# Kernel tuning notes

Measured on AMD Instinct MI355X. Metric: run time of the kernel, lower is better.

The kernel has to match this reference:

```python
import jax, jax.numpy as jnp
import numpy as np

B, T, M, D = 2, 2048, 2048, 128
H = M // D
ROTARY_BASE = 10000
NORM_EPS = 1e-6
QK_SCALE = 1.0 / D  # mult = sqrt(qk_scale) applied to both q and k
INFTY_APPROX = 1e30


def setup_inputs() -> dict:
    key = jax.random.key(0)
    ks = jax.random.split(key, 6)
    w_scale = M ** (-0.5)
    return {
        "x": jax.random.normal(ks[0], (B, T, M), jnp.float32),
        "wq": jax.random.normal(ks[1], (M, H, D), jnp.float32) * w_scale,
        "wk": jax.random.normal(ks[2], (M, H, D), jnp.float32) * w_scale,
        "wv": jax.random.normal(ks[3], (M, H, D), jnp.float32) * w_scale,
        "wo": jax.random.normal(ks[4], (H, D, M), jnp.float32) * w_scale,
        "gq": jnp.zeros((H, 1, D), jnp.float32),
        "bq": jnp.zeros((H, 1, D), jnp.float32),
        "gk": jnp.zeros((H, 1, D), jnp.float32),
        "bk": jnp.zeros((H, 1, D), jnp.float32),
    }


def _qk_layernorm(x, g, b):
    # x: [B,H,T,D]; g,b: [H,1,D]; centered RMS norm with trainable (1+g), b
    x = x - jnp.mean(x, axis=-1, keepdims=True)
    x = x / jnp.sqrt(jnp.mean(jnp.square(x), axis=-1, keepdims=True) + NORM_EPS)
    return x * (1.0 + g)[None] + b[None]


def _rotary(x):
    # x: [B,H,T,D]; half-split rotary encoding
    half = D // 2
    positions = jnp.arange(T, dtype=jnp.float32)[:, None]          # [T,1]
    ang_freqs = jnp.power(float(ROTARY_BASE), -jnp.arange(half, dtype=jnp.float32) / half)[None, :]  # [1,half]
    radians = positions * ang_freqs                                  # [T,half]
    cos = jnp.cos(radians)[None, None].astype(x.dtype)               # [1,1,T,half]
    sin = jnp.sin(radians)[None, None].astype(x.dtype)
    even, odd = jnp.split(x, 2, axis=-1)
    return jnp.concatenate([even * cos - odd * sin, even * sin + odd * cos], axis=-1)


def reference(x, wq, wk, wv, wo, gq, bq, gk, bk):
    q = jnp.einsum('bim,mhd->bhid', x, wq)
    k = jnp.einsum('bim,mhd->bhid', x, wk)
    v = jnp.einsum('bim,mhd->bhid', x, wv)
    q = _rotary(_qk_layernorm(q, gq, bq))
    k = _rotary(_qk_layernorm(k, gk, bk))
    mult = jnp.asarray(QK_SCALE ** 0.5, dtype=x.dtype)
    s = jnp.einsum('bhid,bhjd->bhij', q * mult, k * mult)            # [B,H,T,T]
    i = jnp.arange(T)[:, None]
    j = jnp.arange(T)[None, :]
    future = (i < j)[None, None]                                      # mask future positions
    s = s - jnp.asarray(INFTY_APPROX, dtype=s.dtype) * future
    p = jax.nn.softmax(s, axis=-1)
    o = jnp.einsum('bhij,bhjd->bhid', p, v)
    return jnp.einsum('bhid,hdm->bim', o, wo)
```

## Files before the change

### kernel.cpp

```cpp
#include <hip/hip_runtime.h>


#define NB 2
#define NT 2048
#define NM 2048
#define NH 16
#define ND 128

typedef __attribute__((ext_vector_type(4))) float f32x4;
typedef __attribute__((ext_vector_type(8))) short bf16x8;
typedef __attribute__((ext_vector_type(4))) short bf16x4;

#define AS1 __attribute__((address_space(1)))
#define AS3 __attribute__((address_space(3)))

__device__ __forceinline__ unsigned short f2bf(float f){
  unsigned int u = __float_as_uint(f);
  u = (u + 0x7fffu + ((u >> 16) & 1u)) >> 16;
  return (unsigned short)u;
}
__device__ __forceinline__ float bf2f(short s){
  return __uint_as_float(((unsigned int)(unsigned short)s) << 16);
}
__device__ __forceinline__ float wredsum(float v){
  #pragma unroll
  for (int m = 1; m < 64; m <<= 1) v += __shfl_xor(v, m);
  return v;
}
__device__ __forceinline__ void gload_lds16(const void* g, void* l){
  __builtin_amdgcn_global_load_lds((const AS1 void*)g, (AS3 void*)l, 16, 0, 0);
}

__global__ __launch_bounds__(64) void rope_table_k(float* ctab, float* stab){
  int t = blockIdx.x, i = threadIdx.x;
  float freq = __expf(-(float)i * (9.210340371976184f / 64.0f));
  float ang = (float)t * freq;
  ctab[t * 64 + i] = cosf(ang);
  stab[t * 64 + i] = sinf(ang);
}

__global__ __launch_bounds__(256) void cast_x_k(const float* __restrict__ x,
                                                short* __restrict__ xb){
  size_t gid = (size_t)blockIdx.x * 256 + threadIdx.x;
  float4 v = *(const float4*)(x + gid * 4);
  bf16x4 o;
  o[0] = (short)f2bf(v.x); o[1] = (short)f2bf(v.y);
  o[2] = (short)f2bf(v.z); o[3] = (short)f2bf(v.w);
  *(bf16x4*)(xb + gid * 4) = o;
}

__global__ __launch_bounds__(256) void transpose_w_k(const float* __restrict__ wq,
                                                     const float* __restrict__ wk,
                                                     const float* __restrict__ wv,
                                                     const float* __restrict__ wo,
                                                     short* __restrict__ wT){
  __shared__ float tl[32][33];
  int z = blockIdx.z;
  const float* src = (z == 0) ? wq : (z == 1) ? wk : (z == 2) ? wv : wo;
  short* dst = wT + (size_t)z * 2048 * 2048;
  int n0 = blockIdx.x * 32, k0 = blockIdx.y * 32;
  int cx = threadIdx.x & 31, ry = threadIdx.x >> 5;
  #pragma unroll
  for (int p = 0; p < 4; ++p)
    tl[ry + 8 * p][cx] = src[(size_t)(k0 + ry + 8 * p) * 2048 + n0 + cx];
  __syncthreads();
  #pragma unroll
  for (int p = 0; p < 4; ++p)
    dst[(size_t)(n0 + ry + 8 * p) * 2048 + k0 + cx] =
        (short)f2bf(tl[cx][ry + 8 * p]);
}

#define NKT 32
__global__ __launch_bounds__(512, 2) void gemm256_k(const short* __restrict__ A,
                                                    const short* __restrict__ Bt,
                                                    short* __restrict__ Cq){
  extern __shared__ char lds[];
  const int tid = threadIdx.x;
  const int wid = tid >> 6, lane = tid & 63;
  const int lrow = lane & 15, g8 = lane >> 4;
  const int wm = wid >> 2, wn = wid & 3;
  const int Kdim = 2048;

  int bid = blockIdx.x;
  int s = (bid & 7) * 48 + (bid >> 3);
  const int bx = s & 15;
  const int by = s >> 4;
  const int m0 = bx * 256, n0 = by * 256;

  const int r8 = lane >> 3;
  const int gcol = ((lane & 7) ^ r8) * 8;
  const short* Ab = A  + (size_t)(m0 + wid * 8 + r8) * Kdim + gcol;
  const short* Bb = Bt + (size_t)(n0 + wid * 8 + r8) * Kdim + gcol;

  f32x4 acc[8][4] = {};

  auto STAGE = [&](int c, int kt){
    #pragma unroll
    for (int h = 0; h < 2; ++h)
      #pragma unroll
      for (int l = 0; l < 2; ++l){
        size_t roff = (size_t)(h * 128 + l * 64) * Kdim + kt * 64;
        char* la = lds + c * 32768 + h * 16384 + l * 8192 + wid * 1024;
        gload_lds16(Ab + roff, la);
        gload_lds16(Bb + roff, la + 65536);
      }
  };
  auto ldA = [&](int c, int mi, int kk) -> bf16x8 {
    int row = mi * 16 + lrow;
    int col = (kk * 64 + g8 * 16) ^ ((lrow & 7) << 4);
    return *(const bf16x8*)(lds + c * 32768 + wm * 16384 + row * 128 + col);
  };
  auto ldB = [&](int c, int ni, int kk) -> bf16x8 {
    int row = (wn & 1) * 64 + ni * 16 + lrow;
    int col = (kk * 64 + g8 * 16) ^ ((lrow & 7) << 4);
    return *(const bf16x8*)(lds + 65536 + c * 32768 + (wn >> 1) * 16384 + row * 128 + col);
  };

  STAGE(0, 0);

  for (int kt = 0; kt < NKT; ++kt){
    const int c = kt & 1;
    asm volatile("s_waitcnt vmcnt(0)" ::: "memory");
    __builtin_amdgcn_s_barrier();
    if (kt + 1 < NKT) STAGE(c ^ 1, kt + 1);

    #pragma unroll
    for (int kk = 0; kk < 2; ++kk){
      bf16x8 bfr[4];
      #pragma unroll
      for (int ni = 0; ni < 4; ++ni) bfr[ni] = ldB(c, ni, kk);
      #pragma unroll
      for (int mh = 0; mh < 2; ++mh){
        bf16x8 afr[4];
        #pragma unroll
        for (int mi = 0; mi < 4; ++mi) afr[mi] = ldA(c, mh * 4 + mi, kk);
        #pragma unroll
        for (int mi = 0; mi < 4; ++mi)
          #pragma unroll
          for (int ni = 0; ni < 4; ++ni)
            acc[mh * 4 + mi][ni] = __builtin_amdgcn_mfma_f32_16x16x32_bf16(
                afr[mi], bfr[ni], acc[mh * 4 + mi][ni], 0, 0, 0);
      }
    }
  }

  const int tsel = by >> 3;
  short* dst = Cq + (size_t)tsel * (NB * NH * NT * ND);
  if (tsel < 2){
    #pragma unroll
    for (int mi = 0; mi < 8; ++mi){
      int rowb = m0 + wm * 128 + mi * 16 + g8 * 4;
      #pragma unroll
      for (int ni = 0; ni < 4; ++ni){
        int col = n0 + wn * 64 + ni * 16 + lrow;
        int hd = col & 2047;
        int hh = hd >> 7, d = hd & 127;
        f32x4 a = acc[mi][ni];
        #pragma unroll
        for (int r = 0; r < 4; ++r){
          int bt = rowb + r;
          int b = bt >> 11, t = bt & 2047;
          dst[(((size_t)(b * NH + hh)) * NT + t) * ND + d] = (short)f2bf(a[r]);
        }
      }
    }
  } else {
    #pragma unroll
    for (int mi = 0; mi < 8; ++mi){
      int rowb = m0 + wm * 128 + mi * 16 + g8 * 4;
      int b = rowb >> 11, t0 = rowb & 2047;
      int jb = t0 >> 6, toff = t0 & 63;
      #pragma unroll
      for (int ni = 0; ni < 4; ++ni){
        int col = n0 + wn * 64 + ni * 16 + lrow;
        int hd = col & 2047;
        int hh = hd >> 7, d = hd & 127;
        f32x4 a = acc[mi][ni];
        bf16x4 w4;
        #pragma unroll
        for (int r = 0; r < 4; ++r) w4[r] = (short)f2bf(a[r]);
        *(bf16x4*)&dst[(((size_t)(b * NH + hh) * 32 + jb) * ND + d) * 64 + toff] = w4;
      }
    }
  }
}

__global__ __launch_bounds__(256) void gemm_bt_k(const short* __restrict__ A,
                                                 const short* __restrict__ Bt,
                                                 float* __restrict__ Cout,
                                                 int Kdim){
  __shared__ short As[2][128 * 32];
  __shared__ short Bs[2][128 * 32];
  const int tid = threadIdx.x;
  const int wid = tid >> 6, lane = tid & 63;
  const int lrow = lane & 15, g8 = lane >> 4;
  const int wm = wid >> 1, wn = wid & 1;
  const int m0 = blockIdx.x * 128, n0 = blockIdx.y * 128;
  f32x4 acc[4][4] = {};
  const int srow = lane >> 2;
  const int skcol = (lane & 3) * 8;

  auto STAGE = [&](int c, int kt){
    #pragma unroll
    for (int i = 0; i < 2; ++i){
      int inst = wid * 2 + i;
      int r = inst * 16 + srow;
      const short* sa = A  + (size_t)(m0 + r) * Kdim + kt + skcol;
      const short* sb = Bt + (size_t)(n0 + r) * Kdim + kt + skcol;
      gload_lds16(sa, (char*)As[c] + inst * 1024);
      gload_lds16(sb, (char*)Bs[c] + inst * 1024);
    }
  };

  STAGE(0, 0);
  const int nkt = Kdim >> 5;
  for (int it = 0; it < nkt; ++it){
    const int c = it & 1;
    asm volatile("s_waitcnt vmcnt(0)" ::: "memory");
    __builtin_amdgcn_s_barrier();
    if (it + 1 < nkt) STAGE(c ^ 1, (it + 1) << 5);

    bf16x8 af[4], bfv[4];
    #pragma unroll
    for (int mi = 0; mi < 4; ++mi)
      af[mi] = *(const bf16x8*)&As[c][(wm * 64 + mi * 16 + lrow) * 32 + g8 * 8];
    #pragma unroll
    for (int ni = 0; ni < 4; ++ni)
      bfv[ni] = *(const bf16x8*)&Bs[c][(wn * 64 + ni * 16 + lrow) * 32 + g8 * 8];
    #pragma unroll
    for (int mi = 0; mi < 4; ++mi)
      #pragma unroll
      for (int ni = 0; ni < 4; ++ni)
        acc[mi][ni] = __builtin_amdgcn_mfma_f32_16x16x32_bf16(
            af[mi], bfv[ni], acc[mi][ni], 0, 0, 0);
  }

  #pragma unroll
  for (int mi = 0; mi < 4; ++mi){
    int rowb = m0 + wm * 64 + mi * 16 + g8 * 4;
    #pragma unroll
    for (int ni = 0; ni < 4; ++ni){
      int col = n0 + wn * 64 + ni * 16 + lrow;
      f32x4 a = acc[mi][ni];
      #pragma unroll
      for (int r = 0; r < 4; ++r)
        Cout[(size_t)(rowb + r) * 2048 + col] = a[r];
    }
  }
}

__global__ __launch_bounds__(256) void norm_rope_k(const short* __restrict__ qkv,
                                                   short* __restrict__ outp,
                                                   const float* __restrict__ gq,
                                                   const float* __restrict__ bq,
                                                   const float* __restrict__ gk,
                                                   const float* __restrict__ bk,
                                                   const float* __restrict__ ctab,
                                                   const float* __restrict__ stab){
  int which = blockIdx.y;
  const short* src = qkv + (size_t)which * (NB * NH * NT * ND);
  short* dst = outp + (size_t)which * (NB * NH * NT * ND);
  const float* g = which ? gk : gq;
  const float* bb = which ? bk : bq;
  int wid = threadIdx.x >> 6, lane = threadIdx.x & 63;
  size_t row = (size_t)blockIdx.x * 4 + wid;
  int h = (int)((row >> 11) & 15);
  int t = (int)(row & 2047);
  const short* rp = src + row * ND;
  float v0 = bf2f(rp[lane]), v1 = bf2f(rp[lane + 64]);
  float mean = wredsum(v0 + v1) * (1.0f / 128.0f);
  float c0 = v0 - mean, c1 = v1 - mean;
  float ms = wredsum(c0 * c0 + c1 * c1) * (1.0f / 128.0f);
  float rstd = rsqrtf(ms + 1e-6f);
  float n0 = c0 * rstd * (1.0f + g[h * ND + lane]) + bb[h * ND + lane];
  float n1 = c1 * rstd * (1.0f + g[h * ND + lane + 64]) + bb[h * ND + lane + 64];
  float co = ctab[t * 64 + lane], si = stab[t * 64 + lane];
  short* wp = dst + row * ND;
  wp[lane]      = (short)f2bf(n0 * co - n1 * si);
  wp[lane + 64] = (short)f2bf(n0 * si + n1 * co);
}

__global__ __launch_bounds__(256) void attn_k(const short* __restrict__ qn,
                                              const short* __restrict__ kn,
                                              const short* __restrict__ vt,
                                              short* __restrict__ ob){
  extern __shared__ char lds[];
  const int tid = threadIdx.x;
  const int wid = tid >> 6, lane = tid & 63;
  const int lrow = lane & 15, g8 = lane >> 4;
  const int bh = blockIdx.y;
  const int b = bh >> 4, h = bh & 15;
  const size_t base = (size_t)bh * NT * ND;
  char* Pw = lds + 65536 + wid * 2048;

  auto STAGE = [&](int cb, int jb){
    #pragma unroll
    for (int i = 0; i < 4; ++i){
      int r0 = wid * 16 + i * 4;
      int r = r0 + (lane >> 4);
      int g = lane & 15;
      gload_lds16(kn + base + (size_t)(jb * 64 + r) * ND + ((g ^ (r & 7)) << 3),
                  lds + cb * 16384 + r0 * 256);
    }
    #pragma unroll
    for (int i = 0; i < 4; ++i){
      int d0 = wid * 32 + i * 8;
      int d = d0 + (lane >> 3);
      int g = lane & 7;
      gload_lds16(vt + base + (size_t)jb * 8192 + d * 64 + ((g ^ (d & 7)) << 3),
                  lds + 32768 + cb * 16384 + d0 * 128);
    }
  };

  for (int pass = 0; pass < 2; ++pass){
    const int qt = pass ? (31 - (int)blockIdx.x) : (int)blockIdx.x;
    const int t0 = qt * 64;
    const int tq = t0 + wid * 16 + lrow;
    bf16x8 qf[4];
    #pragma unroll
    for (int dc = 0; dc < 4; ++dc)
      qf[dc] = *(const bf16x8*)(qn + base + (size_t)tq * ND + dc * 32 + g8 * 8);
    f32x4 O[8] = {};
    float m = -3e38f, lsum = 0.0f;
    const int ntiles = qt + 1;

    __syncthreads();
    STAGE(0, 0);

    for (int jb = 0; jb < ntiles; ++jb){
      const int cb = jb & 1;
      asm volatile("s_waitcnt vmcnt(0)" ::: "memory");
      __builtin_amdgcn_s_barrier();
      if (jb + 1 < ntiles) STAGE(cb ^ 1, jb + 1);
      const char* Kb = lds + cb * 16384;
      const char* Vb = lds + 32768 + cb * 16384;

      f32x4 st[4] = {};
      __builtin_amdgcn_s_setprio(1);
      #pragma unroll
      for (int dc = 0; dc < 4; ++dc)
        #pragma unroll
        for (int js = 0; js < 4; ++js){
          int jl = js * 16 + lrow;
          bf16x8 kf = *(const bf16x8*)(Kb + jl * 256 +
                        (((dc * 4 + g8) ^ (jl & 7)) << 4));
          st[js] = __builtin_amdgcn_mfma_f32_16x16x32_bf16(kf, qf[dc], st[js], 0, 0, 0);
        }
      __builtin_amdgcn_s_setprio(0);
      float mx = -3e38f;
      #pragma unroll
      for (int js = 0; js < 4; ++js)
        #pragma unroll
        for (int r = 0; r < 4; ++r){
          float s = st[js][r] * (1.0f / 128.0f);
          int j = jb * 64 + js * 16 + g8 * 4 + r;
          if (j > tq) s = -3e38f;
          st[js][r] = s;
          mx = fmaxf(mx, s);
        }
      mx = fmaxf(mx, __shfl_xor(mx, 16));
      mx = fmaxf(mx, __shfl_xor(mx, 32));
      float mnew = fmaxf(m, mx);
      float fac = __expf(m - mnew);
      m = mnew;
      lsum *= fac;
      #pragma unroll
      for (int dcb = 0; dcb < 8; ++dcb) O[dcb] *= fac;
      float ps = 0.0f;
      #pragma unroll
      for (int js = 0; js < 4; ++js)
        #pragma unroll
        for (int r = 0; r < 4; ++r){
          float p = __expf(st[js][r] - mnew);
          ps += p;
          int jl = js * 16 + g8 * 4 + r;
          *(short*)(Pw + lrow * 128 + ((jl * 2) ^ ((lrow & 7) << 4))) = (short)f2bf(p);
        }
      ps += __shfl_xor(ps, 16);
      ps += __shfl_xor(ps, 32);
      lsum += ps;
      asm volatile("s_waitcnt lgkmcnt(0)" ::: "memory");
      __builtin_amdgcn_s_setprio(1);
      #pragma unroll
      for (int j32 = 0; j32 < 2; ++j32){
        bf16x8 pf = *(const bf16x8*)(Pw + lrow * 128 +
                      ((j32 * 64 + g8 * 16) ^ ((lrow & 7) << 4)));
        #pragma unroll
        for (int dcb = 0; dcb < 8; ++dcb){
          int d = dcb * 16 + lrow;
          bf16x8 vf = *(const bf16x8*)(Vb + d * 128 +
                        (((j32 * 4 + g8) ^ (d & 7)) << 4));
          O[dcb] = __builtin_amdgcn_mfma_f32_16x16x32_bf16(vf, pf, O[dcb], 0, 0, 0);
        }
      }
      __builtin_amdgcn_s_setprio(0);
      __builtin_amdgcn_s_barrier();
    }
    float inv = 1.0f / lsum;
    #pragma unroll
    for (int dcb = 0; dcb < 8; ++dcb){
      bf16x4 w4;
      #pragma unroll
      for (int r = 0; r < 4; ++r) w4[r] = (short)f2bf(O[dcb][r] * inv);
      *(bf16x4*)(ob + ((size_t)(b * NT + tq)) * (NH * ND) + h * ND + dcb * 16 + g8 * 4) = w4;
    }
  }
}

extern "C" void kernel_launch(void* const* d_in, const int* in_sizes, int n_in,
                              void* d_out, int out_size, void* d_ws, size_t ws_size,
                              hipStream_t stream){
  const float* x  = (const float*)d_in[0];
  const float* wq = (const float*)d_in[1];
  const float* wk = (const float*)d_in[2];
  const float* wv = (const float*)d_in[3];
  const float* wo = (const float*)d_in[4];
  const float* gq = (const float*)d_in[5];
  const float* bq = (const float*)d_in[6];
  const float* gk = (const float*)d_in[7];
  const float* bk = (const float*)d_in[8];

  char* ws = (char*)d_ws;
  short* xb   = (short*)(ws);
  short* wT   = (short*)(ws + 16777216);
  short* qkvb = (short*)(ws + 50331648);
  short* qkn  = (short*)(ws + 100663296);
  short* ob   = (short*)(ws + 134217728);
  float* ctab = (float*)(ws + 150994944);
  float* stab = (float*)(ws + 151519232);

  (void)hipFuncSetAttribute((const void*)gemm256_k,
                            hipFuncAttributeMaxDynamicSharedMemorySize, 131072);
  (void)hipFuncSetAttribute((const void*)attn_k,
                            hipFuncAttributeMaxDynamicSharedMemorySize, 73728);

  rope_table_k<<<dim3(2048), dim3(64), 0, stream>>>(ctab, stab);
  cast_x_k<<<dim3(8192), dim3(256), 0, stream>>>(x, xb);
  transpose_w_k<<<dim3(64, 64, 4), dim3(256), 0, stream>>>(wq, wk, wv, wo, wT);
  gemm256_k<<<dim3(384), dim3(512), 131072, stream>>>(xb, wT, qkvb);
  norm_rope_k<<<dim3(16384, 2), dim3(256), 0, stream>>>(qkvb, qkn, gq, bq, gk, bk, ctab, stab);
  attn_k<<<dim3(16, 32), dim3(256), 73728, stream>>>(qkn, qkn + 8388608,
                                                     qkvb + 2 * (size_t)8388608, ob);
  gemm_bt_k<<<dim3(32, 16), dim3(256), 0, stream>>>(ob, wT + 3 * (size_t)4194304,
                                                    (float*)d_out, 2048);
}
```

Measured before the change: 302.0 us.

## Process two query tiles per block to reuse staged K/V tiles

Each attention block now processes two adjacent 64-row query tiles per pass, sharing each staged K/V tile between them, with separate softmax state and P scratch buffers. This halves K/V staging traffic per query and also drops the trailing barrier per iteration. It doubles accumulator registers and raises LDS use, which may reduce occupancy.

```diff
diff --git a/kernel.cpp b/kernel.cpp
--- a/kernel.cpp
+++ b/kernel.cpp
@@ -291,7 +291,8 @@
   const int bh = blockIdx.y;
   const int b = bh >> 4, h = bh & 15;
   const size_t base = (size_t)bh * NT * ND;
-  char* Pw = lds + 65536 + wid * 2048;
+  char* PwA = lds + 65536 + wid * 4096;
+  char* PwB = PwA + 2048;
 
   auto STAGE = [&](int cb, int jb){
     #pragma unroll
@@ -312,17 +313,81 @@
     }
   };
 
+  auto QKSM = [&](const bf16x8* qf, int tq, float& m, float& lsum, f32x4* O,
+                  char* Pw, const char* Kb, int jb){
+    f32x4 st[4] = {};
+    __builtin_amdgcn_s_setprio(1);
+    #pragma unroll
+    for (int dc = 0; dc < 4; ++dc)
+      #pragma unroll
+      for (int js = 0; js < 4; ++js){
+        int jl = js * 16 + lrow;
+        bf16x8 kf = *(const bf16x8*)(Kb + jl * 256 +
+                      (((dc * 4 + g8) ^ (jl & 7)) << 4));
+        st[js] = __builtin_amdgcn_mfma_f32_16x16x32_bf16(kf, qf[dc], st[js], 0, 0, 0);
+      }
+    __builtin_amdgcn_s_setprio(0);
+    float mx = -3e38f;
+    #pragma unroll
+    for (int js = 0; js < 4; ++js)
+      #pragma unroll
+      for (int r = 0; r < 4; ++r){
+        float s = st[js][r] * (1.0f / 128.0f);
+        int j = jb * 64 + js * 16 + g8 * 4 + r;
+        if (j > tq) s = -3e38f;
+        st[js][r] = s;
+        mx = fmaxf(mx, s);
+      }
+    mx = fmaxf(mx, __shfl_xor(mx, 16));
+    mx = fmaxf(mx, __shfl_xor(mx, 32));
+    float mnew = fmaxf(m, mx);
+    float fac = __expf(m - mnew);
+    m = mnew;
+    lsum *= fac;
+    #pragma unroll
+    for (int dcb = 0; dcb < 8; ++dcb) O[dcb] *= fac;
+    float ps = 0.0f;
+    #pragma unroll
+    for (int js = 0; js < 4; ++js)
+      #pragma unroll
+      for (int r = 0; r < 4; ++r){
+        float p = __expf(st[js][r] - mnew);
+        ps += p;
+        int jl = js * 16 + g8 * 4 + r;
+        *(short*)(Pw + lrow * 128 + ((jl * 2) ^ ((lrow & 7) << 4))) = (short)f2bf(p);
+      }
+    ps += __shfl_xor(ps, 16);
+    ps += __shfl_xor(ps, 32);
+    lsum += ps;
+  };
+  auto PV = [&](f32x4* O, const char* Pw, const char* Vb){
+    #pragma unroll
+    for (int j32 = 0; j32 < 2; ++j32){
+      bf16x8 pf = *(const bf16x8*)(Pw + lrow * 128 +
+                    ((j32 * 64 + g8 * 16) ^ ((lrow & 7) << 4)));
+      #pragma unroll
+      for (int dcb = 0; dcb < 8; ++dcb){
+        int d = dcb * 16 + lrow;
+        bf16x8 vf = *(const bf16x8*)(Vb + d * 128 +
+                      (((j32 * 4 + g8) ^ (d & 7)) << 4));
+        O[dcb] = __builtin_amdgcn_mfma_f32_16x16x32_bf16(vf, pf, O[dcb], 0, 0, 0);
+      }
+    }
+  };
+
   for (int pass = 0; pass < 2; ++pass){
-    const int qt = pass ? (31 - (int)blockIdx.x) : (int)blockIdx.x;
-    const int t0 = qt * 64;
-    const int tq = t0 + wid * 16 + lrow;
-    bf16x8 qf[4];
-    #pragma unroll
-    for (int dc = 0; dc < 4; ++dc)
-      qf[dc] = *(const bf16x8*)(qn + base + (size_t)tq * ND + dc * 32 + g8 * 8);
-    f32x4 O[8] = {};
-    float m = -3e38f, lsum = 0.0f;
-    const int ntiles = qt + 1;
+    const int sx = pass ? (15 - (int)blockIdx.x) : (int)blockIdx.x;
+    const int tqA = sx * 128 + wid * 16 + lrow;
+    const int tqB = tqA + 64;
+    bf16x8 qfA[4], qfB[4];
+    #pragma unroll
+    for (int dc = 0; dc < 4; ++dc){
+      qfA[dc] = *(const bf16x8*)(qn + base + (size_t)tqA * ND + dc * 32 + g8 * 8);
+      qfB[dc] = *(const bf16x8*)(qn + base + (size_t)tqB * ND + dc * 32 + g8 * 8);
+    }
+    f32x4 OA[8] = {}, OB[8] = {};
+    float mA = -3e38f, lA = 0.0f, mB = -3e38f, lB = 0.0f;
+    const int ntiles = 2 * sx + 2;
 
     __syncthreads();
     STAGE(0, 0);
@@ -334,75 +399,27 @@
       if (jb + 1 < ntiles) STAGE(cb ^ 1, jb + 1);
       const char* Kb = lds + cb * 16384;
       const char* Vb = lds + 32768 + cb * 16384;
-
-      f32x4 st[4] = {};
-      __builtin_amdgcn_s_setprio(1);
-      #pragma unroll
-      for (int dc = 0; dc < 4; ++dc)
-        #pragma unroll
-        for (int js = 0; js < 4; ++js){
-          int jl = js * 16 + lrow;
-          bf16x8 kf = *(const bf16x8*)(Kb + jl * 256 +
-                        (((dc * 4 + g8) ^ (jl & 7)) << 4));
-          st[js] = __builtin_amdgcn_mfma_f32_16x16x32_bf16(kf, qf[dc], st[js], 0, 0, 0);
-        }
-      __builtin_amdgcn_s_setprio(0);
-      float mx = -3e38f;
-      #pragma unroll
-      for (int js = 0; js < 4; ++js)
-        #pragma unroll
-        for (int r = 0; r < 4; ++r){
-          float s = st[js][r] * (1.0f / 128.0f);
-          int j = jb * 64 + js * 16 + g8 * 4 + r;
-          if (j > tq) s = -3e38f;
-          st[js][r] = s;
-          mx = fmaxf(mx, s);
-        }
-      mx = fmaxf(mx, __shfl_xor(mx, 16));
-      mx = fmaxf(mx, __shfl_xor(mx, 32));
-      float mnew = fmaxf(m, mx);
-      float fac = __expf(m - mnew);
-      m = mnew;
-      lsum *= fac;
-      #pragma unroll
-      for (int dcb = 0; dcb < 8; ++dcb) O[dcb] *= fac;
-      float ps = 0.0f;
-      #pragma unroll
-      for (int js = 0; js < 4; ++js)
-        #pragma unroll
-        for (int r = 0; r < 4; ++r){
-          float p = __expf(st[js][r] - mnew);
-          ps += p;
-          int jl = js * 16 + g8 * 4 + r;
-          *(short*)(Pw + lrow * 128 + ((jl * 2) ^ ((lrow & 7) << 4))) = (short)f2bf(p);
-        }
-      ps += __shfl_xor(ps, 16);
-      ps += __shfl_xor(ps, 32);
-      lsum += ps;
+      const bool Aact = (jb + 1 < ntiles);
+
+      if (Aact) QKSM(qfA, tqA, mA, lA, OA, PwA, Kb, jb);
+      QKSM(qfB, tqB, mB, lB, OB, PwB, Kb, jb);
       asm volatile("s_waitcnt lgkmcnt(0)" ::: "memory");
       __builtin_amdgcn_s_setprio(1);
-      #pragma unroll
-      for (int j32 = 0; j32 < 2; ++j32){
-        bf16x8 pf = *(const bf16x8*)(Pw + lrow * 128 +
-                      ((j32 * 64 + g8 * 16) ^ ((lrow & 7) << 4)));
-        #pragma unroll
-        for (int dcb = 0; dcb < 8; ++dcb){
-          int d = dcb * 16 + lrow;
-          bf16x8 vf = *(const bf16x8*)(Vb + d * 128 +
-                        (((j32 * 4 + g8) ^ (d & 7)) << 4));
-          O[dcb] = __builtin_amdgcn_mfma_f32_16x16x32_bf16(vf, pf, O[dcb], 0, 0, 0);
-        }
-      }
+      if (Aact) PV(OA, PwA, Vb);
+      PV(OB, PwB, Vb);
       __builtin_amdgcn_s_setprio(0);
-      __builtin_amdgcn_s_barrier();
-    }
-    float inv = 1.0f / lsum;
+    }
+    float invA = 1.0f / lA, invB = 1.0f / lB;
     #pragma unroll
     for (int dcb = 0; dcb < 8; ++dcb){
-      bf16x4 w4;
-      #pragma unroll
-      for (int r = 0; r < 4; ++r) w4[r] = (short)f2bf(O[dcb][r] * inv);
-      *(bf16x4*)(ob + ((size_t)(b * NT + tq)) * (NH * ND) + h * ND + dcb * 16 + g8 * 4) = w4;
+      bf16x4 wA, wB;
+      #pragma unroll
+      for (int r = 0; r < 4; ++r){
+        wA[r] = (short)f2bf(OA[dcb][r] * invA);
+        wB[r] = (short)f2bf(OB[dcb][r] * invB);
+      }
+      *(bf16x4*)(ob + ((size_t)(b * NT + tqA)) * (NH * ND) + h * ND + dcb * 16 + g8 * 4) = wA;
+      *(bf16x4*)(ob + ((size_t)(b * NT + tqB)) * (NH * ND) + h * ND + dcb * 16 + g8 * 4) = wB;
     }
   }
 }
@@ -432,14 +449,14 @@
   (void)hipFuncSetAttribute((const void*)gemm256_k,
                             hipFuncAttributeMaxDynamicSharedMemorySize, 131072);
   (void)hipFuncSetAttribute((const void*)attn_k,
-                            hipFuncAttributeMaxDynamicSharedMemorySize, 73728);
+                            hipFuncAttributeMaxDynamicSharedMemorySize, 81920);
 
   rope_table_k<<<dim3(2048), dim3(64), 0, stream>>>(ctab, stab);
   cast_x_k<<<dim3(8192), dim3(256), 0, stream>>>(x, xb);
   transpose_w_k<<<dim3(64, 64, 4), dim3(256), 0, stream>>>(wq, wk, wv, wo, wT);
   gemm256_k<<<dim3(384), dim3(512), 131072, stream>>>(xb, wT, qkvb);
   norm_rope_k<<<dim3(16384, 2), dim3(256), 0, stream>>>(qkvb, qkn, gq, bq, gk, bk, ctab, stab);
-  attn_k<<<dim3(16, 32), dim3(256), 73728, stream>>>(qkn, qkn + 8388608,
+  attn_k<<<dim3(16, 32), dim3(256), 81920, stream>>>(qkn, qkn + 8388608,
                                                      qkvb + 2 * (size_t)8388608, ob);
   gemm_bt_k<<<dim3(32, 16), dim3(256), 0, stream>>>(ob, wT + 3 * (size_t)4194304,
                                                     (float*)d_out, 2048);
```

New measurement: 416.7 us. 38.0% more time.

## Fold softmax scale into Q, use exp2, lazy rescale, skip masked work in attention

Applied to the files above, without the earlier changes.

Q is multiplied in the norm/rope kernel by log2(e)/128, so attention works directly in the base-2 domain with exp2f and no per-element scaling. Inside the loop, masking is applied only on the diagonal tile, and waves whose rows are entirely masked skip the tile. The running max is only updated and O rescaled when the new max exceeds the old one by more than 8. P is packed with v_cvt_pk_bf16_f32 into 8-byte LDS stores, the trailing barrier is removed, and the grid is flattened to 1D with bh in the low bits. Risks are a race on the double buffer now that the trailing barrier is gone, and bf16 P values up to 2^8 from the lazy rescale.

```diff
diff --git a/kernel.cpp b/kernel.cpp
--- a/kernel.cpp
+++ b/kernel.cpp
@@ -262,6 +262,7 @@
   short* dst = outp + (size_t)which * (NB * NH * NT * ND);
   const float* g = which ? gk : gq;
   const float* bb = which ? bk : bq;
+  const float qs = which ? 1.0f : 0.011271055007f;
   int wid = threadIdx.x >> 6, lane = threadIdx.x & 63;
   size_t row = (size_t)blockIdx.x * 4 + wid;
   int h = (int)((row >> 11) & 15);
@@ -276,8 +277,8 @@
   float n1 = c1 * rstd * (1.0f + g[h * ND + lane + 64]) + bb[h * ND + lane + 64];
   float co = ctab[t * 64 + lane], si = stab[t * 64 + lane];
   short* wp = dst + row * ND;
-  wp[lane]      = (short)f2bf(n0 * co - n1 * si);
-  wp[lane + 64] = (short)f2bf(n0 * si + n1 * co);
+  wp[lane]      = (short)f2bf((n0 * co - n1 * si) * qs);
+  wp[lane + 64] = (short)f2bf((n0 * si + n1 * co) * qs);
 }
 
 __global__ __launch_bounds__(256) void attn_k(const short* __restrict__ qn,
@@ -288,7 +289,9 @@
   const int tid = threadIdx.x;
   const int wid = tid >> 6, lane = tid & 63;
   const int lrow = lane & 15, g8 = lane >> 4;
-  const int bh = blockIdx.y;
+  const int id = blockIdx.x;
+  const int qx = id >> 5;
+  const int bh = id & 31;
   const int b = bh >> 4, h = bh & 15;
   const size_t base = (size_t)bh * NT * ND;
   char* Pw = lds + 65536 + wid * 2048;
@@ -313,7 +316,7 @@
   };
 
   for (int pass = 0; pass < 2; ++pass){
-    const int qt = pass ? (31 - (int)blockIdx.x) : (int)blockIdx.x;
+    const int qt = pass ? (31 - qx) : qx;
     const int t0 = qt * 64;
     const int tq = t0 + wid * 16 + lrow;
     bf16x8 qf[4];
@@ -322,79 +325,89 @@
       qf[dc] = *(const bf16x8*)(qn + base + (size_t)tq * ND + dc * 32 + g8 * 8);
     f32x4 O[8] = {};
     float m = -3e38f, lsum = 0.0f;
-    const int ntiles = qt + 1;
 
     __syncthreads();
     STAGE(0, 0);
 
-    for (int jb = 0; jb < ntiles; ++jb){
+    for (int jb = 0; jb <= qt; ++jb){
       const int cb = jb & 1;
       asm volatile("s_waitcnt vmcnt(0)" ::: "memory");
       __builtin_amdgcn_s_barrier();
-      if (jb + 1 < ntiles) STAGE(cb ^ 1, jb + 1);
+      if (jb < qt) STAGE(cb ^ 1, jb + 1);
       const char* Kb = lds + cb * 16384;
       const char* Vb = lds + 32768 + cb * 16384;
 
-      f32x4 st[4] = {};
-      __builtin_amdgcn_s_setprio(1);
-      #pragma unroll
-      for (int dc = 0; dc < 4; ++dc)
+      if (jb * 64 <= t0 + wid * 16 + 15){
+        f32x4 st[4] = {};
+        __builtin_amdgcn_s_setprio(1);
+        #pragma unroll
+        for (int dc = 0; dc < 4; ++dc)
+          #pragma unroll
+          for (int js = 0; js < 4; ++js){
+            int jl = js * 16 + lrow;
+            bf16x8 kf = *(const bf16x8*)(Kb + jl * 256 +
+                          (((dc * 4 + g8) ^ (jl & 7)) << 4));
+            st[js] = __builtin_amdgcn_mfma_f32_16x16x32_bf16(kf, qf[dc], st[js], 0, 0, 0);
+          }
+        __builtin_amdgcn_s_setprio(0);
+        if (jb == qt){
+          #pragma unroll
+          for (int js = 0; js < 4; ++js)
+            #pragma unroll
+            for (int r = 0; r < 4; ++r){
+              int j = jb * 64 + js * 16 + g8 * 4 + r;
+              if (j > tq) st[js][r] = -3e38f;
+            }
+        }
+        f32x4 m4 = st[0];
+        #pragma unroll
+        for (int js = 1; js < 4; ++js)
+          #pragma unroll
+          for (int r = 0; r < 4; ++r) m4[r] = fmaxf(m4[r], st[js][r]);
+        float mx = fmaxf(fmaxf(m4[0], m4[1]), fmaxf(m4[2], m4[3]));
+        mx = fmaxf(mx, __shfl_xor(mx, 16));
+        mx = fmaxf(mx, __shfl_xor(mx, 32));
+        if (!__all(mx <= m + 8.0f)){
+          float mnew = fmaxf(m, mx);
+          float fac = exp2f(m - mnew);
+          m = mnew;
+          lsum *= fac;
+          #pragma unroll
+          for (int dcb = 0; dcb < 8; ++dcb) O[dcb] *= fac;
+        }
+        float ps = 0.0f;
         #pragma unroll
         for (int js = 0; js < 4; ++js){
-          int jl = js * 16 + lrow;
-          bf16x8 kf = *(const bf16x8*)(Kb + jl * 256 +
-                        (((dc * 4 + g8) ^ (jl & 7)) << 4));
-          st[js] = __builtin_amdgcn_mfma_f32_16x16x32_bf16(kf, qf[dc], st[js], 0, 0, 0);
+          float p0 = exp2f(st[js][0] - m);
+          float p1 = exp2f(st[js][1] - m);
+          float p2 = exp2f(st[js][2] - m);
+          float p3 = exp2f(st[js][3] - m);
+          ps += (p0 + p1) + (p2 + p3);
+          unsigned int lo, hi;
+          asm("v_cvt_pk_bf16_f32 %0, %1, %2" : "=v"(lo) : "v"(p0), "v"(p1));
+          asm("v_cvt_pk_bf16_f32 %0, %1, %2" : "=v"(hi) : "v"(p2), "v"(p3));
+          uint2 w; w.x = lo; w.y = hi;
+          *(uint2*)(Pw + lrow * 128 + ((js * 32 + g8 * 8) ^ ((lrow & 7) << 4))) = w;
         }
-      __builtin_amdgcn_s_setprio(0);
-      float mx = -3e38f;
-      #pragma unroll
-      for (int js = 0; js < 4; ++js)
-        #pragma unroll
-        for (int r = 0; r < 4; ++r){
-          float s = st[js][r] * (1.0f / 128.0f);
-          int j = jb * 64 + js * 16 + g8 * 4 + r;
-          if (j > tq) s = -3e38f;
-          st[js][r] = s;
-          mx = fmaxf(mx, s);
+        ps += __shfl_xor(ps, 16);
+        ps += __shfl_xor(ps, 32);
+        lsum += ps;
+        asm volatile("s_waitcnt lgkmcnt(0)" ::: "memory");
+        __builtin_amdgcn_s_setprio(1);
+        #pragma unroll
+        for (int j32 = 0; j32 < 2; ++j32){
+          bf16x8 pf = *(const bf16x8*)(Pw + lrow * 128 +
+                        ((j32 * 64 + g8 * 16) ^ ((lrow & 7) << 4)));
+          #pragma unroll
+          for (int dcb = 0; dcb < 8; ++dcb){
+            int d = dcb * 16 + lrow;
+            bf16x8 vf = *(const bf16x8*)(Vb + d * 128 +
+                          (((j32 * 4 + g8) ^ (d & 7)) << 4));
+            O[dcb] = __builtin_amdgcn_mfma_f32_16x16x32_bf16(vf, pf, O[dcb], 0, 0, 0);
+          }
         }
-      mx = fmaxf(mx, __shfl_xor(mx, 16));
-      mx = fmaxf(mx, __shfl_xor(mx, 32));
-      float mnew = fmaxf(m, mx);
-      float fac = __expf(m - mnew);
-      m = mnew;
-      lsum *= fac;
-      #pragma unroll
-      for (int dcb = 0; dcb < 8; ++dcb) O[dcb] *= fac;
-      float ps = 0.0f;
-      #pragma unroll
-      for (int js = 0; js < 4; ++js)
-        #pragma unroll
-        for (int r = 0; r < 4; ++r){
-          float p = __expf(st[js][r] - mnew);
-          ps += p;
-          int jl = js * 16 + g8 * 4 + r;
-          *(short*)(Pw + lrow * 128 + ((jl * 2) ^ ((lrow & 7) << 4))) = (short)f2bf(p);
-        }
-      ps += __shfl_xor(ps, 16);
-      ps += __shfl_xor(ps, 32);
-      lsum += ps;
-      asm volatile("s_waitcnt lgkmcnt(0)" ::: "memory");
-      __builtin_amdgcn_s_setprio(1);
-      #pragma unroll
-      for (int j32 = 0; j32 < 2; ++j32){
-        bf16x8 pf = *(const bf16x8*)(Pw + lrow * 128 +
-                      ((j32 * 64 + g8 * 16) ^ ((lrow & 7) << 4)));
-        #pragma unroll
-        for (int dcb = 0; dcb < 8; ++dcb){
-          int d = dcb * 16 + lrow;
-          bf16x8 vf = *(const bf16x8*)(Vb + d * 128 +
-                        (((j32 * 4 + g8) ^ (d & 7)) << 4));
-          O[dcb] = __builtin_amdgcn_mfma_f32_16x16x32_bf16(vf, pf, O[dcb], 0, 0, 0);
-        }
+        __builtin_amdgcn_s_setprio(0);
       }
-      __builtin_amdgcn_s_setprio(0);
-      __builtin_amdgcn_s_barrier();
     }
     float inv = 1.0f / lsum;
     #pragma unroll
@@ -439,8 +452,8 @@
   transpose_w_k<<<dim3(64, 64, 4), dim3(256), 0, stream>>>(wq, wk, wv, wo, wT);
   gemm256_k<<<dim3(384), dim3(512), 131072, stream>>>(xb, wT, qkvb);
   norm_rope_k<<<dim3(16384, 2), dim3(256), 0, stream>>>(qkvb, qkn, gq, bq, gk, bk, ctab, stab);
-  attn_k<<<dim3(16, 32), dim3(256), 73728, stream>>>(qkn, qkn + 8388608,
-                                                     qkvb + 2 * (size_t)8388608, ob);
+  attn_k<<<dim3(512), dim3(256), 73728, stream>>>(qkn, qkn + 8388608,
+                                                  qkvb + 2 * (size_t)8388608, ob);
   gemm_bt_k<<<dim3(32, 16), dim3(256), 0, stream>>>(ob, wT + 3 * (size_t)4194304,
                                                     (float*)d_out, 2048);
 }
```

Measured after the change: 285.7 us. -5.4%, faster.
